# Performance work log

Measured on AMD Instinct MI355X. Metric: run time of the kernel, lower is better.

Reference implementation:

```python
import jax, jax.numpy as jnp
import numpy as np

N_NODES = 100000

def setup_inputs() -> dict:
    key = jax.random.key(0)
    k1, k2, k3, k4 = jax.random.split(key, 4)
    feat = jax.random.normal(k1, (N_NODES, 256), dtype=jnp.float32)
    # xavier_uniform for [256,256]: bound = sqrt(6/(256+256))
    bound = float(np.sqrt(6.0 / (256 + 256)))
    weight1 = jax.random.uniform(k2, (256, 256), dtype=jnp.float32, minval=-bound, maxval=bound)
    src = jax.random.randint(k3, (1600000,), 0, N_NODES, dtype=jnp.int64)
    dst = jax.random.randint(k4, (1600000,), 0, N_NODES, dtype=jnp.int64)
    return {"feat": feat, "weight1": weight1, "src": src, "dst": dst}

def reference(feat, weight1, src, dst):
    # Per-etype copy_src + scatter-sum accumulated across etypes == one
    # segment_sum over the union of all edges (norm is computed but unused
    # in the original _apply).
    agg = jax.ops.segment_sum(feat[src], dst, num_segments=N_NODES)  # [N, d]
    h = (agg + feat) @ weight1
    h = jax.nn.relu(h)
    # F.dropout(training=False) is identity
    return h
```

## Files before the change

kernel.cpp:

```cpp
#include <hip/hip_runtime.h>

#define D 256
#define SCAN_THREADS 1024
#define CAP 32
#define MAXOVF 4096
#define BM 64

#define RN 64
#define RSH 6
#define SCAP 2048
#define PCH 8192
#define PTH 512
#define NRANGES_MAX 2048
#define SGT 256

typedef float f32x4 __attribute__((ext_vector_type(4)));
typedef short s16x8 __attribute__((ext_vector_type(8)));

__device__ inline unsigned int f2bf(float x) {
    unsigned int u = __float_as_uint(x);
    return (u + 0x7FFFu + ((u >> 16) & 1u)) >> 16;
}
__device__ inline float bflo(unsigned int u) { return __uint_as_float(u << 16); }
__device__ inline float bfhi(unsigned int u) { return __uint_as_float(u & 0xFFFF0000u); }


__global__ void k_zero(int* __restrict__ p, int n) {
    int i = blockIdx.x * blockDim.x + threadIdx.x;
    if (i < n) p[i] = 0;
}

__global__ __launch_bounds__(256) void k_f2b(const float* __restrict__ f,
                                             unsigned short* __restrict__ fb, long n8) {
    for (long i = blockIdx.x * 256L + threadIdx.x; i < n8; i += (long)gridDim.x * 256) {
        const float4* p = reinterpret_cast<const float4*>(f + i * 8);
        float4 a = p[0], b = p[1];
        uint4 u;
        u.x = f2bf(a.x) | (f2bf(a.y) << 16);
        u.y = f2bf(a.z) | (f2bf(a.w) << 16);
        u.z = f2bf(b.x) | (f2bf(b.y) << 16);
        u.w = f2bf(b.z) | (f2bf(b.w) << 16);
        reinterpret_cast<uint4*>(fb)[i] = u;
    }
}

__global__ __launch_bounds__(256) void k_wTs(const float* __restrict__ W,
                                             unsigned short* __restrict__ wTs) {
    int col = blockIdx.x;
    int k = threadIdx.x;
    unsigned short v = (unsigned short)f2bf(W[(size_t)k * D + col]);
    int ks = k >> 5;
    int byte = ((col << 6) + (((k >> 3) & 3) << 4) + ((k & 7) << 1)) ^ ((col & 7) << 4);
    *reinterpret_cast<unsigned short*>(
        reinterpret_cast<char*>(wTs) + (size_t)ks * 16384 + byte) = v;
}

__global__ __launch_bounds__(PTH) void k_part(const int* __restrict__ src,
                                              const int* __restrict__ dst,
                                              int* __restrict__ gcur,
                                              int* __restrict__ streams,
                                              int* __restrict__ ovf,
                                              int* __restrict__ ovf_cnt,
                                              int E, int nranges) {
    __shared__ int hist[NRANGES_MAX];
    __shared__ int base[NRANGES_MAX];
    __shared__ int off[NRANGES_MAX];
    const int t = threadIdx.x;
    const long e0 = (long)blockIdx.x * PCH;
    for (int i = t; i < nranges; i += PTH) hist[i] = 0;
    __syncthreads();
    int md[PCH / PTH], ms[PCH / PTH];
    #pragma unroll
    for (int i = 0; i < PCH / PTH; ++i) {
        long e = e0 + (long)i * PTH + t;
        if (e < E) {
            md[i] = dst[e];
            ms[i] = src[e];
            atomicAdd(&hist[md[i] >> RSH], 1);
        } else {
            md[i] = -1;
        }
    }
    __syncthreads();
    for (int i = t; i < nranges; i += PTH) {
        int h = hist[i];
        base[i] = h ? atomicAdd(&gcur[i], h) : 0;
        off[i] = 0;
    }
    __syncthreads();
    #pragma unroll
    for (int i = 0; i < PCH / PTH; ++i) {
        if (md[i] >= 0) {
            int r = md[i] >> RSH;
            int p = base[r] + atomicAdd(&off[r], 1);
            if (p < SCAP) {
                streams[(size_t)r * SCAP + p] = (ms[i] << RSH) | (md[i] & (RN - 1));
            } else {
                int o = atomicAdd(ovf_cnt, 1);
                if (o < MAXOVF) { ovf[2 * o] = ms[i]; ovf[2 * o + 1] = md[i]; }
            }
        }
    }
}

__global__ __launch_bounds__(SGT) void k_sg(const unsigned short* __restrict__ featb,
                                            const int* __restrict__ gcur,
                                            const int* __restrict__ streams,
                                            const int* __restrict__ ovf,
                                            const int* __restrict__ ovf_cnt,
                                            unsigned short* __restrict__ aggb, int N) {
    __shared__ int hist[RN], basei[RN], off[RN], scn[RN];
    __shared__ int elist[SCAP];
    const int r = blockIdx.x;
    const int t = threadIdx.x;
    const int node0 = r << RSH;
    int cnt = gcur[r];
    if (cnt > SCAP) cnt = SCAP;
    if (t < RN) { hist[t] = 0; off[t] = 0; }
    __syncthreads();
    int ent[SCAP / SGT];
    #pragma unroll
    for (int i = 0; i < SCAP / SGT; ++i) {
        int p = t + i * SGT;
        if (p < cnt) {
            ent[i] = streams[(size_t)r * SCAP + p];
            atomicAdd(&hist[ent[i] & (RN - 1)], 1);
        } else {
            ent[i] = -1;
        }
    }
    __syncthreads();
    if (t < RN) scn[t] = hist[t];
    __syncthreads();
    for (int st = 1; st < RN; st <<= 1) {
        int v = 0;
        if (t < RN && t >= st) v = scn[t - st];
        __syncthreads();
        if (t < RN) scn[t] += v;
        __syncthreads();
    }
    if (t < RN) basei[t] = scn[t] - hist[t];
    __syncthreads();
    #pragma unroll
    for (int i = 0; i < SCAP / SGT; ++i) {
        if (ent[i] >= 0) {
            int ln_ = ent[i] & (RN - 1);
            int p = basei[ln_] + atomicAdd(&off[ln_], 1);
            elist[p] = ent[i] >> RSH;
        }
    }
    __syncthreads();
    int ovfn = *ovf_cnt;
    if (ovfn > MAXOVF) ovfn = MAXOVF;
    const int wv = t >> 6;
    const int l = t & 63;
    for (int k = 0; k < RN / 4; ++k) {
        int ln_ = wv * (RN / 4) + k;
        int node = node0 + ln_;
        if (node >= N) continue;
        int cb = hist[ln_];
        int bb = basei[ln_];
        uint2 u = reinterpret_cast<const uint2*>(featb + (size_t)node * D)[l];
        float4 acc;
        acc.x = bflo(u.x); acc.y = bfhi(u.x); acc.z = bflo(u.y); acc.w = bfhi(u.y);
        int j = 0;
        for (; j + 16 <= cb; j += 16) {
            int s[16];
            #pragma unroll
            for (int q = 0; q < 16; ++q) s[q] = elist[bb + j + q];
            uint2 v[16];
            #pragma unroll
            for (int q = 0; q < 16; ++q)
                v[q] = reinterpret_cast<const uint2*>(featb + (size_t)s[q] * D)[l];
            #pragma unroll
            for (int q = 0; q < 16; ++q) {
                acc.x += bflo(v[q].x); acc.y += bfhi(v[q].x);
                acc.z += bflo(v[q].y); acc.w += bfhi(v[q].y);
            }
        }
        for (; j + 8 <= cb; j += 8) {
            int s[8];
            #pragma unroll
            for (int q = 0; q < 8; ++q) s[q] = elist[bb + j + q];
            uint2 v[8];
            #pragma unroll
            for (int q = 0; q < 8; ++q)
                v[q] = reinterpret_cast<const uint2*>(featb + (size_t)s[q] * D)[l];
            #pragma unroll
            for (int q = 0; q < 8; ++q) {
                acc.x += bflo(v[q].x); acc.y += bfhi(v[q].x);
                acc.z += bflo(v[q].y); acc.w += bfhi(v[q].y);
            }
        }
        for (; j < cb; ++j) {
            uint2 v = reinterpret_cast<const uint2*>(featb + (size_t)elist[bb + j] * D)[l];
            acc.x += bflo(v.x); acc.y += bfhi(v.x);
            acc.z += bflo(v.y); acc.w += bfhi(v.y);
        }
        if (ovfn > 0) {
            for (int e = 0; e < ovfn; ++e) {
                if (ovf[2 * e + 1] == node) {
                    uint2 v = reinterpret_cast<const uint2*>(featb + (size_t)ovf[2 * e] * D)[l];
                    acc.x += bflo(v.x); acc.y += bfhi(v.x);
                    acc.z += bflo(v.y); acc.w += bfhi(v.y);
                }
            }
        }
        uint2 w;
        w.x = f2bf(acc.x) | (f2bf(acc.y) << 16);
        w.y = f2bf(acc.z) | (f2bf(acc.w) << 16);
        unsigned short* rowp = aggb + (size_t)node * D;
        int us = (l * 4) ^ ((node & 7) << 3);
        *reinterpret_cast<uint2*>(rowp + us) = w;
    }
}

__global__ void k_fillcap(const int* __restrict__ src, const int* __restrict__ dst,
                          int* __restrict__ counts, int* __restrict__ buckets,
                          int* __restrict__ ovf, int* __restrict__ ovf_cnt, int E) {
    for (int e = blockIdx.x * blockDim.x + threadIdx.x; e < E;
         e += gridDim.x * blockDim.x) {
        int d = dst[e];
        int pos = atomicAdd(&counts[d], 1);
        if (pos < CAP) {
            buckets[(size_t)d * CAP + pos] = src[e];
        } else {
            int o = atomicAdd(ovf_cnt, 1);
            if (o < MAXOVF) {
                ovf[2 * o + 0] = src[e];
                ovf[2 * o + 1] = d;
            }
        }
    }
}


#define GAT_BODY(LOAD, ACCUM)                                                  \
    int j = 0;                                                                 \
    for (; j + 16 <= cnt; j += 16) {                                           \
        int s[16];                                                             \
        _Pragma("unroll") for (int q = 0; q < 16; ++q) s[q] = bk[j + q];       \
        LOAD(16)                                                               \
        ACCUM(16)                                                              \
    }                                                                          \
    for (; j + 8 <= cnt; j += 8) {                                             \
        int s[8];                                                              \
        _Pragma("unroll") for (int q = 0; q < 8; ++q) s[q] = bk[j + q];        \
        LOAD(8)                                                                \
        ACCUM(8)                                                               \
    }

__global__ __launch_bounds__(256) void g_bf_aggb(const unsigned short* __restrict__ fb,
                                                 const int* __restrict__ counts,
                                                 const int* __restrict__ buckets,
                                                 const int* __restrict__ ovf,
                                                 const int* __restrict__ ovf_cnt,
                                                 unsigned short* __restrict__ aggb, int N) {
    int node = (int)((blockIdx.x * (long)blockDim.x + threadIdx.x) >> 6);
    int ln = threadIdx.x & 63;
    if (node >= N) return;
    int cnt_raw = counts[node];
    int cnt = cnt_raw > CAP ? CAP : cnt_raw;
    const int* bk = buckets + (size_t)node * CAP;
    uint2 u = reinterpret_cast<const uint2*>(fb + (size_t)node * D)[ln];
    float4 acc;
    acc.x = bflo(u.x); acc.y = bfhi(u.x); acc.z = bflo(u.y); acc.w = bfhi(u.y);
#define BLOAD(W_)                                                              \
    uint2 v[W_];                                                               \
    _Pragma("unroll") for (int q = 0; q < W_; ++q)                             \
        v[q] = reinterpret_cast<const uint2*>(fb + (size_t)s[q] * D)[ln];
#define BACC(W_)                                                               \
    _Pragma("unroll") for (int q = 0; q < W_; ++q) {                           \
        acc.x += bflo(v[q].x); acc.y += bfhi(v[q].x);                          \
        acc.z += bflo(v[q].y); acc.w += bfhi(v[q].y);                          \
    }
    GAT_BODY(BLOAD, BACC)
    for (; j < cnt; ++j) {
        uint2 v = reinterpret_cast<const uint2*>(fb + (size_t)bk[j] * D)[ln];
        acc.x += bflo(v.x); acc.y += bfhi(v.x);
        acc.z += bflo(v.y); acc.w += bfhi(v.y);
    }
    if (cnt_raw > CAP) {
        int m = *ovf_cnt;
        if (m > MAXOVF) m = MAXOVF;
        for (int e = 0; e < m; ++e) {
            if (ovf[2 * e + 1] == node) {
                uint2 v = reinterpret_cast<const uint2*>(fb + (size_t)ovf[2 * e] * D)[ln];
                acc.x += bflo(v.x); acc.y += bfhi(v.x);
                acc.z += bflo(v.y); acc.w += bfhi(v.y);
            }
        }
    }
    uint2 w;
    w.x = f2bf(acc.x) | (f2bf(acc.y) << 16);
    w.y = f2bf(acc.z) | (f2bf(acc.w) << 16);
    unsigned short* rowp = aggb + (size_t)node * D;
    int us = (ln * 4) ^ ((node & 7) << 3);
    *reinterpret_cast<uint2*>(rowp + us) = w;
}

__global__ __launch_bounds__(256) void g_bf_out(const unsigned short* __restrict__ fb,
                                                const int* __restrict__ counts,
                                                const int* __restrict__ buckets,
                                                const int* __restrict__ ovf,
                                                const int* __restrict__ ovf_cnt,
                                                float* __restrict__ out, int N) {
    int node = (int)((blockIdx.x * (long)blockDim.x + threadIdx.x) >> 6);
    int ln = threadIdx.x & 63;
    if (node >= N) return;
    int cnt_raw = counts[node];
    int cnt = cnt_raw > CAP ? CAP : cnt_raw;
    const int* bk = buckets + (size_t)node * CAP;
    uint2 u = reinterpret_cast<const uint2*>(fb + (size_t)node * D)[ln];
    float4 acc;
    acc.x = bflo(u.x); acc.y = bfhi(u.x); acc.z = bflo(u.y); acc.w = bfhi(u.y);
    GAT_BODY(BLOAD, BACC)
    for (; j < cnt; ++j) {
        uint2 v = reinterpret_cast<const uint2*>(fb + (size_t)bk[j] * D)[ln];
        acc.x += bflo(v.x); acc.y += bfhi(v.x);
        acc.z += bflo(v.y); acc.w += bfhi(v.y);
    }
    if (cnt_raw > CAP) {
        int m = *ovf_cnt;
        if (m > MAXOVF) m = MAXOVF;
        for (int e = 0; e < m; ++e) {
            if (ovf[2 * e + 1] == node) {
                uint2 v = reinterpret_cast<const uint2*>(fb + (size_t)ovf[2 * e] * D)[ln];
                acc.x += bflo(v.x); acc.y += bfhi(v.x);
                acc.z += bflo(v.y); acc.w += bfhi(v.y);
            }
        }
    }
    reinterpret_cast<float4*>(out + (size_t)node * D)[ln] = acc;
}

__global__ __launch_bounds__(256) void g_f32_out(const float* __restrict__ feat,
                                                 const int* __restrict__ counts,
                                                 const int* __restrict__ buckets,
                                                 const int* __restrict__ ovf,
                                                 const int* __restrict__ ovf_cnt,
                                                 float* __restrict__ out, int N) {
    int node = (int)((blockIdx.x * (long)blockDim.x + threadIdx.x) >> 6);
    int ln = threadIdx.x & 63;
    if (node >= N) return;
    int cnt_raw = counts[node];
    int cnt = cnt_raw > CAP ? CAP : cnt_raw;
    const int* bk = buckets + (size_t)node * CAP;
    float4 acc = reinterpret_cast<const float4*>(feat + (size_t)node * D)[ln];
#define FLOAD(W_)                                                              \
    float4 v[W_];                                                              \
    _Pragma("unroll") for (int q = 0; q < W_; ++q)                             \
        v[q] = reinterpret_cast<const float4*>(feat + (size_t)s[q] * D)[ln];
#define FACC(W_)                                                               \
    _Pragma("unroll") for (int q = 0; q < W_; ++q) {                           \
        acc.x += v[q].x; acc.y += v[q].y; acc.z += v[q].z; acc.w += v[q].w;    \
    }
    GAT_BODY(FLOAD, FACC)
    for (; j < cnt; ++j) {
        float4 v = reinterpret_cast<const float4*>(feat + (size_t)bk[j] * D)[ln];
        acc.x += v.x; acc.y += v.y; acc.z += v.z; acc.w += v.w;
    }
    if (cnt_raw > CAP) {
        int m = *ovf_cnt;
        if (m > MAXOVF) m = MAXOVF;
        for (int e = 0; e < m; ++e) {
            if (ovf[2 * e + 1] == node) {
                float4 v = reinterpret_cast<const float4*>(feat + (size_t)ovf[2 * e] * D)[ln];
                acc.x += v.x; acc.y += v.y; acc.z += v.z; acc.w += v.w;
            }
        }
    }
    reinterpret_cast<float4*>(out + (size_t)node * D)[ln] = acc;
}


__global__ void k_hist(const int* __restrict__ dst, int* __restrict__ counts, int E) {
    for (int e = blockIdx.x * blockDim.x + threadIdx.x; e < E;
         e += gridDim.x * blockDim.x)
        atomicAdd(&counts[dst[e]], 1);
}

__global__ __launch_bounds__(SCAN_THREADS) void k_scan(const int* __restrict__ counts,
                                                       int* __restrict__ offsets,
                                                       int* __restrict__ cursor,
                                                       int N) {
    __shared__ int s[SCAN_THREADS];
    const int t = threadIdx.x;
    const int chunk = (N + SCAN_THREADS - 1) / SCAN_THREADS;
    const int lo = t * chunk;
    const int hi = min(N, lo + chunk);
    int local = 0;
    for (int i = lo; i < hi; ++i) local += counts[i];
    s[t] = local;
    __syncthreads();
    for (int str = 1; str < SCAN_THREADS; str <<= 1) {
        int v = (t >= str) ? s[t - str] : 0;
        __syncthreads();
        s[t] += v;
        __syncthreads();
    }
    int run = s[t] - local;
    for (int i = lo; i < hi; ++i) {
        offsets[i] = run;
        cursor[i] = run;
        run += counts[i];
    }
    if (t == SCAN_THREADS - 1) offsets[N] = s[SCAN_THREADS - 1];
}

__global__ void k_fill(const int* __restrict__ src, const int* __restrict__ dst,
                       int* __restrict__ cursor, int* __restrict__ buckets, int E) {
    for (int e = blockIdx.x * blockDim.x + threadIdx.x; e < E;
         e += gridDim.x * blockDim.x) {
        int pos = atomicAdd(&cursor[dst[e]], 1);
        buckets[pos] = src[e];
    }
}

__global__ __launch_bounds__(256) void k_gather_csr(const float* __restrict__ feat,
                                                    const int* __restrict__ offsets,
                                                    const int* __restrict__ buckets,
                                                    float* __restrict__ out, int N) {
    int wave = (int)((blockIdx.x * (long)blockDim.x + threadIdx.x) >> 6);
    int lane = threadIdx.x & 63;
    if (wave >= N) return;
    const int off = offsets[wave];
    const int end = offsets[wave + 1];
    float4 acc = reinterpret_cast<const float4*>(feat + (size_t)wave * D)[lane];
    int j = off;
    for (; j + 8 <= end; j += 8) {
        int s[8];
        #pragma unroll
        for (int q = 0; q < 8; ++q) s[q] = buckets[j + q];
        float4 v[8];
        #pragma unroll
        for (int q = 0; q < 8; ++q)
            v[q] = reinterpret_cast<const float4*>(feat + (size_t)s[q] * D)[lane];
        #pragma unroll
        for (int q = 0; q < 8; ++q) {
            acc.x += v[q].x; acc.y += v[q].y; acc.z += v[q].z; acc.w += v[q].w;
        }
    }
    for (; j < end; ++j) {
        float4 v = reinterpret_cast<const float4*>(feat + (size_t)buckets[j] * D)[lane];
        acc.x += v.x; acc.y += v.y; acc.z += v.z; acc.w += v.w;
    }
    reinterpret_cast<float4*>(out + (size_t)wave * D)[lane] = acc;
}


__global__ __launch_bounds__(256) void gc_copy(const float* __restrict__ feat,
                                               float* __restrict__ agg, long n4) {
    long i = (long)blockIdx.x * blockDim.x + threadIdx.x;
    if (i < n4)
        reinterpret_cast<float4*>(agg)[i] = reinterpret_cast<const float4*>(feat)[i];
}

__global__ __launch_bounds__(256) void gc_scatter(const float* __restrict__ feat,
                                                  const int* __restrict__ src,
                                                  const int* __restrict__ dst,
                                                  float* __restrict__ agg, int n_edges) {
    int wave = (int)((blockIdx.x * (long)blockDim.x + threadIdx.x) >> 6);
    int lane = threadIdx.x & 63;
    if (wave >= n_edges) return;
    int s = src[wave];
    int d = dst[wave];
    const float4 v = reinterpret_cast<const float4*>(feat + (size_t)s * D)[lane];
    float* p = agg + (size_t)d * D + (size_t)lane * 4;
    atomicAdd(p + 0, v.x);
    atomicAdd(p + 1, v.y);
    atomicAdd(p + 2, v.z);
    atomicAdd(p + 3, v.w);
}


__device__ inline void gload16(const char* g, const unsigned char* lds) {
    __builtin_amdgcn_global_load_lds(
        (const __attribute__((address_space(1))) void*)g,
        (__attribute__((address_space(3))) void*)lds, 16, 0, 0);
}

__global__ __launch_bounds__(256) void gemm_mfma_b(const unsigned short* __restrict__ aggb,
                                                   const unsigned short* __restrict__ wTs,
                                                   float* __restrict__ out, int n_rows) {
    __shared__ __align__(16) unsigned char s_a[BM * 512];
    __shared__ __align__(16) unsigned char s_b[16384];
    const int t = threadIdx.x;
    const int row0 = blockIdx.x * BM;
    const int wv = t >> 6;
    const int l = t & 63;
    const char* wb = reinterpret_cast<const char*>(wTs);

    const char* gbase = reinterpret_cast<const char*>(aggb) + (size_t)row0 * 512;
    #pragma unroll
    for (int q = 0; q < 8; ++q) {
        int off = wv * 8192 + q * 1024;
        gload16(gbase + off + l * 16, s_a + off);
    }
    #pragma unroll
    for (int i = 0; i < 4; ++i) {
        int off = wv * 4096 + i * 1024;
        gload16(wb + off + l * 16, s_b + off);
    }
    __syncthreads();

    f32x4 acc[16];
    #pragma unroll
    for (int ct = 0; ct < 16; ++ct) acc[ct] = (f32x4){0.f, 0.f, 0.f, 0.f};

    const int lr = wv * 16 + (l & 15);
    const int g = l >> 4;
    for (int ks = 0; ks < 8; ++ks) {
        const int kb = ks * 32 + g * 8;
        const int ab = (lr * 512 + kb * 2) ^ ((lr & 7) << 4);
        s16x8 af = *reinterpret_cast<const s16x8*>(s_a + ab);
        #pragma unroll
        for (int ct = 0; ct < 16; ++ct) {
            int col = ct * 16 + (l & 15);
            int bb = (col * 64 + g * 16) ^ ((col & 7) << 4);
            s16x8 bf = *reinterpret_cast<const s16x8*>(s_b + bb);
            acc[ct] = __builtin_amdgcn_mfma_f32_16x16x32_bf16(af, bf, acc[ct], 0, 0, 0);
        }
        __syncthreads();
        if (ks < 7) {
            #pragma unroll
            for (int i = 0; i < 4; ++i) {
                int off = wv * 4096 + i * 1024;
                gload16(wb + (size_t)(ks + 1) * 16384 + off + l * 16, s_b + off);
            }
            __syncthreads();
        }
    }

    const int rbase = row0 + wv * 16 + (l >> 4) * 4;
    const int cb = l & 15;
    #pragma unroll
    for (int ct = 0; ct < 16; ++ct) {
        #pragma unroll
        for (int r = 0; r < 4; ++r) {
            int row = rbase + r;
            if (row < n_rows)
                out[(size_t)row * D + ct * 16 + cb] = fmaxf(acc[ct][r], 0.f);
        }
    }
}

__global__ __launch_bounds__(256) void gemm_mfma(const unsigned short* __restrict__ wTs,
                                                 float* __restrict__ out, int n_rows) {
    __shared__ __align__(16) unsigned char s_a[BM * 512];
    __shared__ __align__(16) unsigned char s_b[16384];
    const int t = threadIdx.x;
    const int row0 = blockIdx.x * BM;
    const int wv = t >> 6;
    const int l = t & 63;
    const char* wb = reinterpret_cast<const char*>(wTs);

    #pragma unroll
    for (int i = 0; i < 4; ++i) {
        int off = wv * 4096 + i * 1024;
        gload16(wb + off + l * 16, s_b + off);
    }
    #pragma unroll
    for (int i = 0; i < 16; ++i) {
        int f4 = t + 256 * i;
        int row = f4 >> 6;
        int kc = f4 & 63;
        int grow = row0 + row;
        if (grow >= n_rows) grow = n_rows - 1;
        float4 v = *reinterpret_cast<const float4*>(out + (size_t)grow * D + kc * 4);
        uint2 u;
        u.x = f2bf(v.x) | (f2bf(v.y) << 16);
        u.y = f2bf(v.z) | (f2bf(v.w) << 16);
        int byte = (row * 512 + kc * 8) ^ ((row & 7) << 4);
        *reinterpret_cast<uint2*>(s_a + byte) = u;
    }
    __syncthreads();

    f32x4 acc[16];
    #pragma unroll
    for (int ct = 0; ct < 16; ++ct) acc[ct] = (f32x4){0.f, 0.f, 0.f, 0.f};

    const int lr = wv * 16 + (l & 15);
    const int g = l >> 4;
    for (int ks = 0; ks < 8; ++ks) {
        const int kb = ks * 32 + g * 8;
        const int ab = (lr * 512 + kb * 2) ^ ((lr & 7) << 4);
        s16x8 af = *reinterpret_cast<const s16x8*>(s_a + ab);
        #pragma unroll
        for (int ct = 0; ct < 16; ++ct) {
            int col = ct * 16 + (l & 15);
            int bb = (col * 64 + g * 16) ^ ((col & 7) << 4);
            s16x8 bf = *reinterpret_cast<const s16x8*>(s_b + bb);
            acc[ct] = __builtin_amdgcn_mfma_f32_16x16x32_bf16(af, bf, acc[ct], 0, 0, 0);
        }
        __syncthreads();
        if (ks < 7) {
            #pragma unroll
            for (int i = 0; i < 4; ++i) {
                int off = wv * 4096 + i * 1024;
                gload16(wb + (size_t)(ks + 1) * 16384 + off + l * 16, s_b + off);
            }
            __syncthreads();
        }
    }

    const int rbase = row0 + wv * 16 + (l >> 4) * 4;
    const int cb = l & 15;
    #pragma unroll
    for (int ct = 0; ct < 16; ++ct) {
        #pragma unroll
        for (int r = 0; r < 4; ++r) {
            int row = rbase + r;
            if (row < n_rows)
                out[(size_t)row * D + ct * 16 + cb] = fmaxf(acc[ct][r], 0.f);
        }
    }
}

__global__ __launch_bounds__(256) void gemm_relu(const float* __restrict__ Wm,
                                                 float* __restrict__ out, int n_rows) {
    __shared__ float s_a[32][D];
    const int row0 = blockIdx.x * 32;
    const int c = threadIdx.x;
    {
        const float4* gsrc = reinterpret_cast<const float4*>(out + (size_t)row0 * D);
        float4* ldst = reinterpret_cast<float4*>(&s_a[0][0]);
        #pragma unroll
        for (int i = 0; i < 8; ++i)
            ldst[threadIdx.x + i * 256] = gsrc[threadIdx.x + i * 256];
    }
    __syncthreads();
    float acc[32];
    #pragma unroll
    for (int r = 0; r < 32; ++r) acc[r] = 0.f;
    #pragma unroll 4
    for (int k = 0; k < D; ++k) {
        float w = Wm[(size_t)k * D + c];
        #pragma unroll
        for (int r = 0; r < 32; ++r) acc[r] += s_a[r][k] * w;
    }
    #pragma unroll
    for (int r = 0; r < 32; ++r) {
        int row = row0 + r;
        if (row < n_rows) out[(size_t)row * D + c] = fmaxf(acc[r], 0.f);
    }
}

extern "C" void kernel_launch(void* const* d_in, const int* in_sizes, int n_in,
                              void* d_out, int out_size, void* d_ws, size_t ws_size,
                              hipStream_t stream) {
    const float* feat = (const float*)d_in[0];
    const float* W    = (const float*)d_in[1];
    const int*   src  = (const int*)d_in[2];
    const int*   dst  = (const int*)d_in[3];
    float* out = (float*)d_out;

    const int N = in_sizes[0] / D;
    const int E = in_sizes[2];
    const int Npad = ((N + BM - 1) / BM) * BM;
    auto al = [](size_t x) { return (x + 255) & ~(size_t)255; };

    const int nranges = (N + RN - 1) / RN;
    const int gemm_blocks = (N + BM - 1) / BM;
    const int gat_blocks = (N + 3) / 4;

    const size_t hdr_bytes   = ((size_t)nranges + 1 + 2 * MAXOVF) * 4;
    const size_t strm_off    = al(hdr_bytes);
    const size_t strm_sz     = (size_t)nranges * SCAP * 4;
    const size_t a2_featb_off = al(strm_off + strm_sz);
    const size_t featb_sz    = (size_t)N * D * 2;
    const size_t a2_wt_off   = al(a2_featb_off + featb_sz);
    const size_t wt_sz       = (size_t)D * D * 2;
    const size_t a2_aggb_off = al(a2_wt_off + wt_sz);
    const size_t aggb_sz     = (size_t)Npad * D * 2;
    const size_t need_A2     = a2_aggb_off + aggb_sz;

    const size_t cap_bytes = ((size_t)N + 1 + 2 * MAXOVF + (size_t)N * CAP) * 4;
    const size_t featb_off = al(cap_bytes);
    const size_t wt_off    = al(featb_off + featb_sz);
    const size_t aggb_off  = al(wt_off + wt_sz);
    const size_t need_A    = aggb_off + aggb_sz;
    const size_t need_B    = wt_off + wt_sz;
    const size_t need_C    = cap_bytes;
    const size_t need_csr  = ((size_t)3 * N + 1 + (size_t)E) * 4;

    if (ws_size >= need_A2 && nranges <= NRANGES_MAX) {
        char* base = (char*)d_ws;
        int* gcur    = (int*)base;
        int* ovf_cnt = gcur + nranges;
        int* ovf     = ovf_cnt + 1;
        int* streams = (int*)(base + strm_off);
        unsigned short* featb = (unsigned short*)(base + a2_featb_off);
        unsigned short* wTs   = (unsigned short*)(base + a2_wt_off);
        unsigned short* aggb  = (unsigned short*)(base + a2_aggb_off);

        k_zero<<<(nranges + 1 + 255) / 256, 256, 0, stream>>>(gcur, nranges + 1);
        k_f2b<<<2048, 256, 0, stream>>>(feat, featb, (long)N * D / 8);
        k_wTs<<<D, 256, 0, stream>>>(W, wTs);
        k_part<<<(E + PCH - 1) / PCH, PTH, 0, stream>>>(src, dst, gcur, streams,
                                                        ovf, ovf_cnt, E, nranges);
        k_sg<<<nranges, SGT, 0, stream>>>(featb, gcur, streams, ovf, ovf_cnt, aggb, N);
        gemm_mfma_b<<<gemm_blocks, 256, 0, stream>>>(aggb, wTs, out, N);
    } else if (ws_size >= need_C) {
        char* base = (char*)d_ws;
        int* counts  = (int*)base;
        int* ovf_cnt = counts + N;
        int* ovf     = ovf_cnt + 1;
        int* buckets = ovf + 2 * MAXOVF;

        k_zero<<<(N + 1 + 255) / 256, 256, 0, stream>>>(counts, N + 1);

        if (ws_size >= need_A) {
            unsigned short* featb = (unsigned short*)(base + featb_off);
            unsigned short* wTs   = (unsigned short*)(base + wt_off);
            unsigned short* aggb  = (unsigned short*)(base + aggb_off);
            k_f2b<<<2048, 256, 0, stream>>>(feat, featb, (long)N * D / 8);
            k_wTs<<<D, 256, 0, stream>>>(W, wTs);
            k_fillcap<<<2048, 256, 0, stream>>>(src, dst, counts, buckets, ovf, ovf_cnt, E);
            g_bf_aggb<<<gat_blocks, 256, 0, stream>>>(featb, counts, buckets, ovf, ovf_cnt, aggb, N);
            gemm_mfma_b<<<gemm_blocks, 256, 0, stream>>>(aggb, wTs, out, N);
        } else if (ws_size >= need_B) {
            unsigned short* featb = (unsigned short*)(base + featb_off);
            unsigned short* wTs   = (unsigned short*)(base + wt_off);
            k_f2b<<<2048, 256, 0, stream>>>(feat, featb, (long)N * D / 8);
            k_wTs<<<D, 256, 0, stream>>>(W, wTs);
            k_fillcap<<<2048, 256, 0, stream>>>(src, dst, counts, buckets, ovf, ovf_cnt, E);
            g_bf_out<<<gat_blocks, 256, 0, stream>>>(featb, counts, buckets, ovf, ovf_cnt, out, N);
            gemm_mfma<<<gemm_blocks, 256, 0, stream>>>(wTs, out, N);
        } else {
            unsigned short* wTs = (unsigned short*)(((uintptr_t)buckets + 255) & ~(uintptr_t)255);
            k_fillcap<<<2048, 256, 0, stream>>>(src, dst, counts, buckets, ovf, ovf_cnt, E);
            g_f32_out<<<gat_blocks, 256, 0, stream>>>(feat, counts, buckets, ovf, ovf_cnt, out, N);
            k_wTs<<<D, 256, 0, stream>>>(W, wTs);
            gemm_mfma<<<gemm_blocks, 256, 0, stream>>>(wTs, out, N);
        }
    } else if (ws_size >= need_csr) {
        int* counts  = (int*)d_ws;
        int* offsets = counts + N;
        int* cursor  = offsets + N + 1;
        int* buckets = cursor + N;

        k_zero<<<(N + 255) / 256, 256, 0, stream>>>(counts, N);
        k_hist<<<2048, 256, 0, stream>>>(dst, counts, E);
        k_scan<<<1, SCAN_THREADS, 0, stream>>>(counts, offsets, cursor, N);
        k_fill<<<2048, 256, 0, stream>>>(src, dst, cursor, buckets, E);
        k_gather_csr<<<gat_blocks, 256, 0, stream>>>(feat, offsets, buckets, out, N);
        unsigned short* wTs =
            (unsigned short*)(((uintptr_t)buckets + 255) & ~(uintptr_t)255);
        k_wTs<<<D, 256, 0, stream>>>(W, wTs);
        gemm_mfma<<<gemm_blocks, 256, 0, stream>>>(wTs, out, N);
    } else {
        long n4 = (long)N * D / 4;
        gc_copy<<<(int)((n4 + 255) / 256), 256, 0, stream>>>(feat, out, n4);
        gc_scatter<<<(E + 3) / 4, 256, 0, stream>>>(feat, src, dst, out, E);
        gemm_relu<<<(N + 31) / 32, 256, 0, stream>>>(W, out, N);
    }
}
```

Measured before the change: 254.1 us.

## Fuse preprocessing kernels and halve partition range size for scatter-gather

Merges the zeroing of range cursors, the weight transpose/bf16 swizzle, and the feature fp32-to-bf16 conversion into one kernel launch, removing two launches and their serialization gaps on the main path. It also halves the node range per partition (RN 64 to 32, SCAP 2048 to 1024) and doubles the maximum number of ranges, giving the scatter-gather kernel more, smaller blocks. Several unused fallback paths (CSR, fp32-output bf16 gather) are removed. Smaller ranges increase parallelism but may raise overflow frequency and partition overhead.

```diff
diff --git a/kernel.cpp b/kernel.cpp
--- a/kernel.cpp
+++ b/kernel.cpp
@@ -6,12 +6,12 @@
 #define MAXOVF 4096
 #define BM 64
 
-#define RN 64
-#define RSH 6
-#define SCAP 2048
+#define RN 32
+#define RSH 5
+#define SCAP 1024
 #define PCH 8192
 #define PTH 512
-#define NRANGES_MAX 2048
+#define NRANGES_MAX 4096
 #define SGT 256
 
 typedef float f32x4 __attribute__((ext_vector_type(4)));
@@ -23,6 +23,35 @@
 }
 __device__ inline float bflo(unsigned int u) { return __uint_as_float(u << 16); }
 __device__ inline float bfhi(unsigned int u) { return __uint_as_float(u & 0xFFFF0000u); }
+
+__global__ __launch_bounds__(256) void k_pre(const float* __restrict__ feat,
+                                             unsigned short* __restrict__ featb,
+                                             const float* __restrict__ W,
+                                             unsigned short* __restrict__ wTs,
+                                             int* __restrict__ gcur, int nz, long n8) {
+    const int bid = blockIdx.x;
+    const int t = threadIdx.x;
+    if (bid < 256) {
+        unsigned short v = (unsigned short)f2bf(W[(size_t)t * D + bid]);
+        int ks = t >> 5;
+        int byte = ((bid << 6) + (((t >> 3) & 3) << 4) + ((t & 7) << 1)) ^ ((bid & 7) << 4);
+        *reinterpret_cast<unsigned short*>(
+            reinterpret_cast<char*>(wTs) + (size_t)ks * 16384 + byte) = v;
+    } else if (bid < 272) {
+        int i = (bid - 256) * 256 + t;
+        if (i < nz) gcur[i] = 0;
+    }
+    for (long i = bid * 256L + t; i < n8; i += (long)gridDim.x * 256) {
+        const float4* p = reinterpret_cast<const float4*>(feat + i * 8);
+        float4 a = p[0], b = p[1];
+        uint4 u;
+        u.x = f2bf(a.x) | (f2bf(a.y) << 16);
+        u.y = f2bf(a.z) | (f2bf(a.w) << 16);
+        u.z = f2bf(b.x) | (f2bf(b.y) << 16);
+        u.w = f2bf(b.z) | (f2bf(b.w) << 16);
+        reinterpret_cast<uint4*>(featb)[i] = u;
+    }
+}
 
 
 __global__ void k_zero(int* __restrict__ p, int n) {
@@ -299,41 +328,6 @@
     *reinterpret_cast<uint2*>(rowp + us) = w;
 }
 
-__global__ __launch_bounds__(256) void g_bf_out(const unsigned short* __restrict__ fb,
-                                                const int* __restrict__ counts,
-                                                const int* __restrict__ buckets,
-                                                const int* __restrict__ ovf,
-                                                const int* __restrict__ ovf_cnt,
-                                                float* __restrict__ out, int N) {
-    int node = (int)((blockIdx.x * (long)blockDim.x + threadIdx.x) >> 6);
-    int ln = threadIdx.x & 63;
-    if (node >= N) return;
-    int cnt_raw = counts[node];
-    int cnt = cnt_raw > CAP ? CAP : cnt_raw;
-    const int* bk = buckets + (size_t)node * CAP;
-    uint2 u = reinterpret_cast<const uint2*>(fb + (size_t)node * D)[ln];
-    float4 acc;
-    acc.x = bflo(u.x); acc.y = bfhi(u.x); acc.z = bflo(u.y); acc.w = bfhi(u.y);
-    GAT_BODY(BLOAD, BACC)
-    for (; j < cnt; ++j) {
-        uint2 v = reinterpret_cast<const uint2*>(fb + (size_t)bk[j] * D)[ln];
-        acc.x += bflo(v.x); acc.y += bfhi(v.x);
-        acc.z += bflo(v.y); acc.w += bfhi(v.y);
-    }
-    if (cnt_raw > CAP) {
-        int m = *ovf_cnt;
-        if (m > MAXOVF) m = MAXOVF;
-        for (int e = 0; e < m; ++e) {
-            if (ovf[2 * e + 1] == node) {
-                uint2 v = reinterpret_cast<const uint2*>(fb + (size_t)ovf[2 * e] * D)[ln];
-                acc.x += bflo(v.x); acc.y += bfhi(v.x);
-                acc.z += bflo(v.y); acc.w += bfhi(v.y);
-            }
-        }
-    }
-    reinterpret_cast<float4*>(out + (size_t)node * D)[ln] = acc;
-}
-
 __global__ __launch_bounds__(256) void g_f32_out(const float* __restrict__ feat,
                                                  const int* __restrict__ counts,
                                                  const int* __restrict__ buckets,
@@ -374,81 +368,6 @@
 }
 
 
-__global__ void k_hist(const int* __restrict__ dst, int* __restrict__ counts, int E) {
-    for (int e = blockIdx.x * blockDim.x + threadIdx.x; e < E;
-         e += gridDim.x * blockDim.x)
-        atomicAdd(&counts[dst[e]], 1);
-}
-
-__global__ __launch_bounds__(SCAN_THREADS) void k_scan(const int* __restrict__ counts,
-                                                       int* __restrict__ offsets,
-                                                       int* __restrict__ cursor,
-                                                       int N) {
-    __shared__ int s[SCAN_THREADS];
-    const int t = threadIdx.x;
-    const int chunk = (N + SCAN_THREADS - 1) / SCAN_THREADS;
-    const int lo = t * chunk;
-    const int hi = min(N, lo + chunk);
-    int local = 0;
-    for (int i = lo; i < hi; ++i) local += counts[i];
-    s[t] = local;
-    __syncthreads();
-    for (int str = 1; str < SCAN_THREADS; str <<= 1) {
-        int v = (t >= str) ? s[t - str] : 0;
-        __syncthreads();
-        s[t] += v;
-        __syncthreads();
-    }
-    int run = s[t] - local;
-    for (int i = lo; i < hi; ++i) {
-        offsets[i] = run;
-        cursor[i] = run;
-        run += counts[i];
-    }
-    if (t == SCAN_THREADS - 1) offsets[N] = s[SCAN_THREADS - 1];
-}
-
-__global__ void k_fill(const int* __restrict__ src, const int* __restrict__ dst,
-                       int* __restrict__ cursor, int* __restrict__ buckets, int E) {
-    for (int e = blockIdx.x * blockDim.x + threadIdx.x; e < E;
-         e += gridDim.x * blockDim.x) {
-        int pos = atomicAdd(&cursor[dst[e]], 1);
-        buckets[pos] = src[e];
-    }
-}
-
-__global__ __launch_bounds__(256) void k_gather_csr(const float* __restrict__ feat,
-                                                    const int* __restrict__ offsets,
-                                                    const int* __restrict__ buckets,
-                                                    float* __restrict__ out, int N) {
-    int wave = (int)((blockIdx.x * (long)blockDim.x + threadIdx.x) >> 6);
-    int lane = threadIdx.x & 63;
-    if (wave >= N) return;
-    const int off = offsets[wave];
-    const int end = offsets[wave + 1];
-    float4 acc = reinterpret_cast<const float4*>(feat + (size_t)wave * D)[lane];
-    int j = off;
-    for (; j + 8 <= end; j += 8) {
-        int s[8];
-        #pragma unroll
-        for (int q = 0; q < 8; ++q) s[q] = buckets[j + q];
-        float4 v[8];
-        #pragma unroll
-        for (int q = 0; q < 8; ++q)
-            v[q] = reinterpret_cast<const float4*>(feat + (size_t)s[q] * D)[lane];
-        #pragma unroll
-        for (int q = 0; q < 8; ++q) {
-            acc.x += v[q].x; acc.y += v[q].y; acc.z += v[q].z; acc.w += v[q].w;
-        }
-    }
-    for (; j < end; ++j) {
-        float4 v = reinterpret_cast<const float4*>(feat + (size_t)buckets[j] * D)[lane];
-        acc.x += v.x; acc.y += v.y; acc.z += v.z; acc.w += v.w;
-    }
-    reinterpret_cast<float4*>(out + (size_t)wave * D)[lane] = acc;
-}
-
-
 __global__ __launch_bounds__(256) void gc_copy(const float* __restrict__ feat,
                                                float* __restrict__ agg, long n4) {
     long i = (long)blockIdx.x * blockDim.x + threadIdx.x;
@@ -680,9 +599,6 @@
     const size_t wt_off    = al(featb_off + featb_sz);
     const size_t aggb_off  = al(wt_off + wt_sz);
     const size_t need_A    = aggb_off + aggb_sz;
-    const size_t need_B    = wt_off + wt_sz;
-    const size_t need_C    = cap_bytes;
-    const size_t need_csr  = ((size_t)3 * N + 1 + (size_t)E) * 4;
 
     if (ws_size >= need_A2 && nranges <= NRANGES_MAX) {
         char* base = (char*)d_ws;
@@ -694,59 +610,39 @@
         unsigned short* wTs   = (unsigned short*)(base + a2_wt_off);
         unsigned short* aggb  = (unsigned short*)(base + a2_aggb_off);
 
-        k_zero<<<(nranges + 1 + 255) / 256, 256, 0, stream>>>(gcur, nranges + 1);
-        k_f2b<<<2048, 256, 0, stream>>>(feat, featb, (long)N * D / 8);
-        k_wTs<<<D, 256, 0, stream>>>(W, wTs);
+        k_pre<<<2048, 256, 0, stream>>>(feat, featb, W, wTs, gcur, nranges + 1,
+                                        (long)N * D / 8);
         k_part<<<(E + PCH - 1) / PCH, PTH, 0, stream>>>(src, dst, gcur, streams,
                                                         ovf, ovf_cnt, E, nranges);
         k_sg<<<nranges, SGT, 0, stream>>>(featb, gcur, streams, ovf, ovf_cnt, aggb, N);
         gemm_mfma_b<<<gemm_blocks, 256, 0, stream>>>(aggb, wTs, out, N);
-    } else if (ws_size >= need_C) {
+    } else if (ws_size >= need_A) {
         char* base = (char*)d_ws;
         int* counts  = (int*)base;
         int* ovf_cnt = counts + N;
         int* ovf     = ovf_cnt + 1;
         int* buckets = ovf + 2 * MAXOVF;
+        unsigned short* featb = (unsigned short*)(base + featb_off);
+        unsigned short* wTs   = (unsigned short*)(base + wt_off);
+        unsigned short* aggb  = (unsigned short*)(base + aggb_off);
 
         k_zero<<<(N + 1 + 255) / 256, 256, 0, stream>>>(counts, N + 1);
-
-        if (ws_size >= need_A) {
-            unsigned short* featb = (unsigned short*)(base + featb_off);
-            unsigned short* wTs   = (unsigned short*)(base + wt_off);
-            unsigned short* aggb  = (unsigned short*)(base + aggb_off);
-            k_f2b<<<2048, 256, 0, stream>>>(feat, featb, (long)N * D / 8);
-            k_wTs<<<D, 256, 0, stream>>>(W, wTs);
-            k_fillcap<<<2048, 256, 0, stream>>>(src, dst, counts, buckets, ovf, ovf_cnt, E);
-            g_bf_aggb<<<gat_blocks, 256, 0, stream>>>(featb, counts, buckets, ovf, ovf_cnt, aggb, N);
-            gemm_mfma_b<<<gemm_blocks, 256, 0, stream>>>(aggb, wTs, out, N);
-        } else if (ws_size >= need_B) {
-            unsigned short* featb = (unsigned short*)(base + featb_off);
-            unsigned short* wTs   = (unsigned short*)(base + wt_off);
-            k_f2b<<<2048, 256, 0, stream>>>(feat, featb, (long)N * D / 8);
-            k_wTs<<<D, 256, 0, stream>>>(W, wTs);
-            k_fillcap<<<2048, 256, 0, stream>>>(src, dst, counts, buckets, ovf, ovf_cnt, E);
-            g_bf_out<<<gat_blocks, 256, 0, stream>>>(featb, counts, buckets, ovf, ovf_cnt, out, N);
-            gemm_mfma<<<gemm_blocks, 256, 0, stream>>>(wTs, out, N);
-        } else {
-            unsigned short* wTs = (unsigned short*)(((uintptr_t)buckets + 255) & ~(uintptr_t)255);
-            k_fillcap<<<2048, 256, 0, stream>>>(src, dst, counts, buckets, ovf, ovf_cnt, E);
-            g_f32_out<<<gat_blocks, 256, 0, stream>>>(feat, counts, buckets, ovf, ovf_cnt, out, N);
-            k_wTs<<<D, 256, 0, stream>>>(W, wTs);
-            gemm_mfma<<<gemm_blocks, 256, 0, stream>>>(wTs, out, N);
-        }
-    } else if (ws_size >= need_csr) {
-        int* counts  = (int*)d_ws;
-        int* offsets = counts + N;
-        int* cursor  = offsets + N + 1;
-        int* buckets = cursor + N;
-
-        k_zero<<<(N + 255) / 256, 256, 0, stream>>>(counts, N);
-        k_hist<<<2048, 256, 0, stream>>>(dst, counts, E);
-        k_scan<<<1, SCAN_THREADS, 0, stream>>>(counts, offsets, cursor, N);
-        k_fill<<<2048, 256, 0, stream>>>(src, dst, cursor, buckets, E);
-        k_gather_csr<<<gat_blocks, 256, 0, stream>>>(feat, offsets, buckets, out, N);
-        unsigned short* wTs =
-            (unsigned short*)(((uintptr_t)buckets + 255) & ~(uintptr_t)255);
+        k_f2b<<<2048, 256, 0, stream>>>(feat, featb, (long)N * D / 8);
+        k_wTs<<<D, 256, 0, stream>>>(W, wTs);
+        k_fillcap<<<2048, 256, 0, stream>>>(src, dst, counts, buckets, ovf, ovf_cnt, E);
+        g_bf_aggb<<<gat_blocks, 256, 0, stream>>>(featb, counts, buckets, ovf, ovf_cnt, aggb, N);
+        gemm_mfma_b<<<gemm_blocks, 256, 0, stream>>>(aggb, wTs, out, N);
+    } else if (ws_size >= cap_bytes) {
+        char* base = (char*)d_ws;
+        int* counts  = (int*)base;
+        int* ovf_cnt = counts + N;
+        int* ovf     = ovf_cnt + 1;
+        int* buckets = ovf + 2 * MAXOVF;
+        unsigned short* wTs = (unsigned short*)(((uintptr_t)buckets + 255) & ~(uintptr_t)255);
+
+        k_zero<<<(N + 1 + 255) / 256, 256, 0, stream>>>(counts, N + 1);
+        k_fillcap<<<2048, 256, 0, stream>>>(src, dst, counts, buckets, ovf, ovf_cnt, E);
+        g_f32_out<<<gat_blocks, 256, 0, stream>>>(feat, counts, buckets, ovf, ovf_cnt, out, N);
         k_wTs<<<D, 256, 0, stream>>>(W, wTs);
         gemm_mfma<<<gemm_blocks, 256, 0, stream>>>(wTs, out, N);
     } else {
```

New measurement: 231.1 us. 1.1x faster.
